# Kernel optimization log

Measured on AMD Instinct MI355X. Metric: run time of the kernel, lower is better.

## Reference

```python
import jax, jax.numpy as jnp
import numpy as np

N, D, H, DK, DEG = 8192, 512, 8, 64, 16
E = N * DEG
M = N


def setup_inputs() -> dict:
    key = jax.random.key(0)
    ks = jax.random.split(key, 12)
    x = jax.random.normal(ks[0], (N, D), dtype=jnp.float32)
    # every node has DEG neighbors -> sorted row index, random cols
    row_index = jnp.repeat(jnp.arange(N, dtype=jnp.int64), DEG)
    col_index = jax.random.randint(ks[1], (E,), 0, M, dtype=jnp.int64)
    to_col_index = jax.random.randint(ks[2], (M,), 0, N, dtype=jnp.int64)
    att_bias = 0.1 * jax.random.normal(ks[3], (H, E), dtype=jnp.float32)
    pos = 10.0 * jax.random.uniform(ks[4], (N, 3), dtype=jnp.float32)
    col_pos = 10.0 * jax.random.uniform(ks[5], (M, 3), dtype=jnp.float32)
    dist = jnp.linalg.norm(col_pos[col_index] - pos[row_index], axis=-1)
    s = 1.0 / np.sqrt(D)
    Wq = s * jax.random.normal(ks[6], (H, DK, D), dtype=jnp.float32)
    Wqv = s * jax.random.normal(ks[7], (H, 3, D), dtype=jnp.float32)
    Wk = s * jax.random.normal(ks[8], (H, DK, D), dtype=jnp.float32)
    Wv = s * jax.random.normal(ks[9], (H, DK, D), dtype=jnp.float32)
    Wout = s * jax.random.normal(ks[10], (D, D + 4 * H), dtype=jnp.float32)
    bout = jnp.zeros((D,), dtype=jnp.float32)
    return {"x": x, "row_index": row_index, "col_index": col_index,
            "to_col_index": to_col_index, "att_bias": att_bias, "dist": dist,
            "pos": pos, "col_pos": col_pos, "Wq": Wq, "Wqv": Wqv, "Wk": Wk,
            "Wv": Wv, "Wout": Wout, "bout": bout}


def reference(x, row_index, col_index, to_col_index, att_bias, dist, pos,
              col_pos, Wq, Wqv, Wk, Wv, Wout, bout):
    n = x.shape[0]
    dk = Wq.shape[1]
    scale = 1.0 / jnp.sqrt(jnp.asarray(dk, x.dtype))
    # per-head projections: [H, N, dk]
    q = jnp.einsum('nd,hkd->hnk', x, Wq) * scale
    qv = jnp.einsum('nd,hkd->hnk', x, Wqv)              # [H, N, 3]
    kx = jnp.einsum('nd,hkd->hnk', x, Wk)[:, to_col_index]  # [H, M, dk]
    vx = jnp.einsum('nd,hkd->hnk', x, Wv)[:, to_col_index]
    # gather per edge -> [E, H, *]
    qe = q[:, row_index].transpose(1, 0, 2)
    ke = kx[:, col_index].transpose(1, 0, 2)
    qve = qv[:, row_index].transpose(1, 0, 2)           # [E, H, 3]
    rel = col_pos[col_index] - pos[row_index]           # [E, 3]
    dist_e = jnp.where(dist == 0, jnp.inf, dist)        # masked_fill(dist==0, inf)
    # angular = qv_row . col_pos_col - qv_row . pos_row = qv_row . rel
    angular = jnp.einsum('ehc,ec->eh', qve, rel)
    logit = jnp.einsum('ehk,ehk->eh', qe, ke) + att_bias.T + angular / dist_e[:, None]
    # sparse (per-row segment) softmax
    m = jax.ops.segment_max(logit, row_index, num_segments=n)
    p = jnp.exp(logit - m[row_index])
    s = jax.ops.segment_sum(p, row_index, num_segments=n)
    att = p / s[row_index]                              # [E, H]
    natt = att / dist_e[:, None]
    dst_vec = jax.ops.segment_sum(natt[:, :, None] * col_pos[col_index][:, None, :],
                                  row_index, num_segments=n)   # [N, H, 3]
    avg_inv_dist = jax.ops.segment_sum(natt, row_index, num_segments=n)  # [N, H]
    src_vec = avg_inv_dist[:, :, None] * pos[:, None, :]
    diff = dst_vec - src_vec
    feat3 = diff / jnp.maximum(jnp.linalg.norm(diff, axis=-1, keepdims=True), 1e-12)
    ve = vx[:, col_index].transpose(1, 0, 2)            # [E, H, dk]
    y = jax.ops.segment_sum(att[:, :, None] * ve, row_index, num_segments=n)  # [N, H, dk]
    feat = jnp.concatenate([y, feat3, avg_inv_dist[:, :, None]], axis=-1)
    feat = feat.reshape(n, -1)                          # [N, H*(dk+4)]
    return feat @ Wout.T + bout
```

## Files before the change

### kernel.cpp

```cpp
#include <hip/hip_runtime.h>
#include <math.h>

#define N_NODES 8192
#define D_FEAT  512
#define DEG     16
#define E_EDGES (N_NODES * DEG)
#define FEAT_W  576
#define FEAT_USED 544
#define OUT_W   512
#define QKV_W   1664

typedef unsigned short u16;
typedef __attribute__((ext_vector_type(8))) short short8;
typedef __attribute__((ext_vector_type(8))) unsigned short us8;
typedef __attribute__((ext_vector_type(4))) float f32x4;

__device__ __forceinline__ u16 f2bf(float f) {
    union { float f; unsigned u; } c; c.f = f;
    unsigned u = c.u;
    unsigned r = u + 0x7FFFu + ((u >> 16) & 1u);
    return (u16)(r >> 16);
}
__device__ __forceinline__ float bf2f(u16 h) {
    union { unsigned u; float f; } c; c.u = ((unsigned)h) << 16;
    return c.f;
}

__device__ __forceinline__ void async16(const void* g, void* l) {
    __builtin_amdgcn_global_load_lds(
        (const __attribute__((address_space(1))) void*)g,
        (__attribute__((address_space(3))) void*)l, 16, 0, 0);
}

__device__ __forceinline__ us8 pack8(float4 a, float4 b, float s) {
    us8 w;
    w[0] = f2bf(a.x * s); w[1] = f2bf(a.y * s);
    w[2] = f2bf(a.z * s); w[3] = f2bf(a.w * s);
    w[4] = f2bf(b.x * s); w[5] = f2bf(b.y * s);
    w[6] = f2bf(b.z * s); w[7] = f2bf(b.w * s);
    return w;
}

__global__ __launch_bounds__(256) void gemm_qkv(
    const float* __restrict__ x,
    const float* __restrict__ Wq, const float* __restrict__ Wk,
    const float* __restrict__ Wv, const float* __restrict__ Wqv,
    u16* __restrict__ qkv)
{
    __shared__ u16 smem[128 * 64 * 2];
    u16* sA = smem;
    u16* sB = smem + 128 * 64;

    const int tid = threadIdx.x;
    const int flat = blockIdx.x;
    const int xcd = flat & 7;
    const int rr  = flat >> 3;
    const int bm  = (xcd + 8 * (rr / 13)) * 128;
    const int bn  = (rr % 13) * 128;

    const int wave = tid >> 6;
    const int lane = tid & 63;
    const int wr   = (wave >> 1) * 64;
    const int wc   = (wave & 1) * 64;
    const int lrow = lane & 15;
    const int quad = lane >> 4;

    f32x4 acc[4][4];
    #pragma unroll
    for (int i = 0; i < 4; ++i)
        #pragma unroll
        for (int j = 0; j < 4; ++j) {
            f32x4 z = {0.f, 0.f, 0.f, 0.f};
            acc[i][j] = z;
        }

    for (int k0 = 0; k0 < 512; k0 += 64) {
        #pragma unroll
        for (int i = 0; i < 4; ++i) {
            const int lin = i * 256 + tid;
            const int row = lin >> 3;
            const int seg = ((lin & 7) ^ (row & 7)) << 3;
            {
                const float* s = x + (size_t)(bm + row) * 512 + k0 + seg;
                const float4 a0 = *(const float4*)(s);
                const float4 a1 = *(const float4*)(s + 4);
                *(us8*)&sA[lin << 3] = pack8(a0, a1, 1.f);
            }
            {
                const int br = bn + row;
                const float* s = nullptr; float sc = 1.f;
                if (br < 512)       { s = Wq + (size_t)br * 512; sc = 0.125f; }
                else if (br < 1024) { s = Wk + (size_t)(br - 512) * 512; }
                else if (br < 1536) { s = Wv + (size_t)(br - 1024) * 512; }
                else if (br < 1560) { s = Wqv + (size_t)(br - 1536) * 512; }
                us8 w = {0, 0, 0, 0, 0, 0, 0, 0};
                if (s) {
                    const float4 b0 = *(const float4*)(s + k0 + seg);
                    const float4 b1 = *(const float4*)(s + k0 + seg + 4);
                    w = pack8(b0, b1, sc);
                }
                *(us8*)&sB[lin << 3] = w;
            }
        }
        __syncthreads();

        #pragma unroll
        for (int ko = 0; ko < 64; ko += 32) {
            const int cbase = ko >> 3;
            short8 a_h[4], b_h[4];
            #pragma unroll
            for (int t = 0; t < 4; ++t) {
                const int ra = wr + t * 16 + lrow;
                const int rb = wc + t * 16 + lrow;
                a_h[t] = *(const short8*)&sA[ra * 64 + (((cbase + quad) ^ (ra & 7)) << 3)];
                b_h[t] = *(const short8*)&sB[rb * 64 + (((cbase + quad) ^ (rb & 7)) << 3)];
            }
            #pragma unroll
            for (int mt = 0; mt < 4; ++mt)
                #pragma unroll
                for (int nt = 0; nt < 4; ++nt)
                    acc[mt][nt] = __builtin_amdgcn_mfma_f32_16x16x32_bf16(
                        a_h[mt], b_h[nt], acc[mt][nt], 0, 0, 0);
        }
        __syncthreads();
    }

    #pragma unroll
    for (int nt = 0; nt < 4; ++nt) {
        const int col = bn + wc + nt * 16 + lrow;
        #pragma unroll
        for (int mt = 0; mt < 4; ++mt)
            #pragma unroll
            for (int r = 0; r < 4; ++r) {
                const int row = bm + wr + mt * 16 + quad * 4 + r;
                qkv[(size_t)row * QKV_W + col] = f2bf(acc[mt][nt][r]);
            }
    }
}

__global__ __launch_bounds__(256) void gemm_out(
    const u16* __restrict__ feat, const float* __restrict__ Wout,
    const float* __restrict__ bout, float* __restrict__ out)
{
    __shared__ u16 smem[128 * 64 * 2];
    u16* sA = smem;
    u16* sB = smem + 128 * 64;

    const int tid = threadIdx.x;
    const int flat = blockIdx.x;
    const int xcd = flat & 7;
    const int rr  = flat >> 3;
    const int bm  = (xcd + 8 * (rr / 4)) * 128;
    const int bn  = (rr % 4) * 128;

    const int wave = tid >> 6;
    const int lane = tid & 63;
    const int wr   = (wave >> 1) * 64;
    const int wc   = (wave & 1) * 64;
    const int lrow = lane & 15;
    const int quad = lane >> 4;

    f32x4 acc[4][4];
    #pragma unroll
    for (int i = 0; i < 4; ++i)
        #pragma unroll
        for (int j = 0; j < 4; ++j) {
            f32x4 z = {0.f, 0.f, 0.f, 0.f};
            acc[i][j] = z;
        }

    for (int k0 = 0; k0 < FEAT_W; k0 += 64) {
        #pragma unroll
        for (int i = 0; i < 4; ++i) {
            const int lin = i * 256 + tid;
            const int row = lin >> 3;
            const int seg = ((lin & 7) ^ (row & 7)) << 3;
            async16(feat + (size_t)(bm + row) * FEAT_W + k0 + seg, sA + (lin << 3));
            {
                const int col = k0 + seg;
                us8 w = {0, 0, 0, 0, 0, 0, 0, 0};
                if (col < FEAT_USED) {
                    const float* s = Wout + (size_t)(bn + row) * FEAT_USED + col;
                    const float4 b0 = *(const float4*)(s);
                    const float4 b1 = *(const float4*)(s + 4);
                    w = pack8(b0, b1, 1.f);
                }
                *(us8*)&sB[lin << 3] = w;
            }
        }
        __syncthreads();

        #pragma unroll
        for (int ko = 0; ko < 64; ko += 32) {
            const int cbase = ko >> 3;
            short8 a_h[4], b_h[4];
            #pragma unroll
            for (int t = 0; t < 4; ++t) {
                const int ra = wr + t * 16 + lrow;
                const int rb = wc + t * 16 + lrow;
                a_h[t] = *(const short8*)&sA[ra * 64 + (((cbase + quad) ^ (ra & 7)) << 3)];
                b_h[t] = *(const short8*)&sB[rb * 64 + (((cbase + quad) ^ (rb & 7)) << 3)];
            }
            #pragma unroll
            for (int mt = 0; mt < 4; ++mt)
                #pragma unroll
                for (int nt = 0; nt < 4; ++nt)
                    acc[mt][nt] = __builtin_amdgcn_mfma_f32_16x16x32_bf16(
                        a_h[mt], b_h[nt], acc[mt][nt], 0, 0, 0);
        }
        __syncthreads();
    }

    #pragma unroll
    for (int nt = 0; nt < 4; ++nt) {
        const int col = bn + wc + nt * 16 + lrow;
        const float bb = bout[col];
        #pragma unroll
        for (int mt = 0; mt < 4; ++mt)
            #pragma unroll
            for (int r = 0; r < 4; ++r) {
                const int row = bm + wr + mt * 16 + quad * 4 + r;
                out[(size_t)row * OUT_W + col] = acc[mt][nt][r] + bb;
            }
    }
}

#define EK_WAVES 2
__global__ __launch_bounds__(EK_WAVES * 64) void edge_kernel(
    const u16* __restrict__ qkv,
    const int* __restrict__ col_index, const int* __restrict__ to_col,
    const float* __restrict__ att_bias, const float* __restrict__ dist,
    const float* __restrict__ pos, const float* __restrict__ col_pos,
    u16* __restrict__ feat)
{
    __shared__ u16 vbuf[EK_WAVES * DEG * 512];

    const int wave = threadIdx.x >> 6;
    const int lane = threadIdx.x & 63;
    const int n = blockIdx.x * EK_WAVES + wave;
    const int h = lane >> 3;
    const int sub = lane & 7;

    const size_t qbase = (size_t)n * QKV_W;
    const int hoff = lane * 8;

    float qf[8];
    {
        const us8 qu = *(const us8*)(qkv + qbase + hoff);
        #pragma unroll
        for (int i = 0; i < 8; ++i) qf[i] = bf2f(qu[i]);
    }
    float qv0, qv1, qv2;
    {
        const float qvl = bf2f(qkv[qbase + 1536 + (lane < 24 ? lane : 0)]);
        qv0 = __shfl(qvl, h * 3 + 0);
        qv1 = __shfl(qvl, h * 3 + 1);
        qv2 = __shfl(qvl, h * 3 + 2);
    }
    const float px = pos[3 * n + 0], py = pos[3 * n + 1], pz = pos[3 * n + 2];

    const int j16 = lane & 15;
    const int e0  = n * DEG + j16;
    const int c_l  = col_index[e0];
    const int cc_l = to_col[c_l];
    const float d_l = dist[e0];
    const float invd_l = (d_l == 0.f) ? 0.f : (1.f / d_l);
    const float rx_l = col_pos[3 * c_l + 0] - px;
    const float ry_l = col_pos[3 * c_l + 1] - py;
    const float rz_l = col_pos[3 * c_l + 2] - pz;

    const float b0 = att_bias[(size_t)h * E_EDGES + n * DEG + sub * 2 + 0];
    const float b1 = att_bias[(size_t)h * E_EDGES + n * DEG + sub * 2 + 1];

    float logit[DEG];
    u16* vb = &vbuf[wave * DEG * 512];
    #pragma unroll
    for (int j = 0; j < DEG; ++j) {
        const int cc = __shfl(cc_l, j);
        const u16* rowp = qkv + (size_t)cc * QKV_W + hoff;
        async16(rowp + 1024, vb + j * 512);
        const us8 ku = *(const us8*)(rowp + 512);
        float dot = 0.f;
        #pragma unroll
        for (int i = 0; i < 8; ++i) dot += qf[i] * bf2f(ku[i]);
        dot += __shfl_xor(dot, 1, 8);
        dot += __shfl_xor(dot, 2, 8);
        dot += __shfl_xor(dot, 4, 8);
        const float invd = __shfl(invd_l, j);
        const float ang = qv0 * __shfl(rx_l, j) + qv1 * __shfl(ry_l, j)
                        + qv2 * __shfl(rz_l, j);
        const float bj = __shfl((j & 1) ? b1 : b0, j >> 1, 8);
        logit[j] = dot + bj + ang * invd;
    }

    float m = logit[0];
    #pragma unroll
    for (int j = 1; j < DEG; ++j) m = fmaxf(m, logit[j]);
    float s = 0.f;
    #pragma unroll
    for (int j = 0; j < DEG; ++j) { logit[j] = __expf(logit[j] - m); s += logit[j]; }
    const float inv_s = 1.f / s;

    __syncthreads();

    float y[8] = {0.f, 0.f, 0.f, 0.f, 0.f, 0.f, 0.f, 0.f};
    float dx = 0.f, dy = 0.f, dz = 0.f, aid = 0.f;
    #pragma unroll
    for (int j = 0; j < DEG; ++j) {
        const float a = logit[j] * inv_s;
        const us8 vu = *(const us8*)&vb[j * 512 + hoff];
        #pragma unroll
        for (int i = 0; i < 8; ++i) y[i] += a * bf2f(vu[i]);
        const float na = a * __shfl(invd_l, j);
        dx += na * __shfl(rx_l, j);
        dy += na * __shfl(ry_l, j);
        dz += na * __shfl(rz_l, j);
        aid += na;
    }

    u16* f = feat + (size_t)n * FEAT_W + h * 68;
    ushort4 o0, o1;
    o0.x = f2bf(y[0]); o0.y = f2bf(y[1]); o0.z = f2bf(y[2]); o0.w = f2bf(y[3]);
    o1.x = f2bf(y[4]); o1.y = f2bf(y[5]); o1.z = f2bf(y[6]); o1.w = f2bf(y[7]);
    *(ushort4*)(f + sub * 8 + 0) = o0;
    *(ushort4*)(f + sub * 8 + 4) = o1;
    if (sub == 0) {
        const float nrm = sqrtf(dx * dx + dy * dy + dz * dz);
        const float rn = 1.f / fmaxf(nrm, 1e-12f);
        ushort4 ex;
        ex.x = f2bf(dx * rn); ex.y = f2bf(dy * rn);
        ex.z = f2bf(dz * rn); ex.w = f2bf(aid);
        *(ushort4*)(f + 64) = ex;
    }
}

extern "C" void kernel_launch(void* const* d_in, const int* in_sizes, int n_in,
                              void* d_out, int out_size, void* d_ws, size_t ws_size,
                              hipStream_t stream)
{
    const float* x         = (const float*)d_in[0];
    const int*   col_index = (const int*)d_in[2];
    const int*   to_col    = (const int*)d_in[3];
    const float* att_bias  = (const float*)d_in[4];
    const float* dist      = (const float*)d_in[5];
    const float* pos       = (const float*)d_in[6];
    const float* col_pos   = (const float*)d_in[7];
    const float* Wq        = (const float*)d_in[8];
    const float* Wqv       = (const float*)d_in[9];
    const float* Wk        = (const float*)d_in[10];
    const float* Wv        = (const float*)d_in[11];
    const float* Wout      = (const float*)d_in[12];
    const float* bout      = (const float*)d_in[13];
    float* out = (float*)d_out;

    char* ws = (char*)d_ws;
    u16* qkv  = (u16*)(ws + 0);
    u16* feat = (u16*)(ws + 27262976);

    dim3 blk(256);

    hipLaunchKernelGGL(gemm_qkv, dim3(64 * 13), blk, 0, stream,
                       x, Wq, Wk, Wv, Wqv, qkv);

    hipLaunchKernelGGL(edge_kernel, dim3(N_NODES / EK_WAVES), dim3(EK_WAVES * 64),
                       0, stream,
                       qkv, col_index, to_col, att_bias, dist, pos, col_pos, feat);

    hipLaunchKernelGGL(gemm_out, dim3(64 * 4), blk, 0, stream,
                       feat, Wout, bout, out);
}
```

Measured before the change: 197.6 us.

## Pre-convert GEMM operands to bf16 in a prep kernel and use async LDS loads

Adds a prep kernel that converts x, the fused Wq/Wk/Wv matrix and a zero-padded Wout to bf16 once per call. It also computes the small qv projection in fp32 there, so the QKV GEMM drops from 13 to 12 column tiles. Both GEMMs now stream bf16 tiles straight into LDS with global_load_lds instead of loading fp32 and converting in registers, which cuts redundant per-tile conversion and halves operand bytes. gemm_out uses 64-row M tiles to double its block count from 256 to 512. The cost is an extra launch and an extra round trip of the bf16 copies through memory.

```diff
diff --git a/kernel.cpp b/kernel.cpp
--- a/kernel.cpp
+++ b/kernel.cpp
@@ -8,7 +8,7 @@
 #define FEAT_W  576
 #define FEAT_USED 544
 #define OUT_W   512
-#define QKV_W   1664
+#define QKV_W   1536
 
 typedef unsigned short u16;
 typedef __attribute__((ext_vector_type(8))) short short8;
@@ -32,19 +32,8 @@
         (__attribute__((address_space(3))) void*)l, 16, 0, 0);
 }
 
-__device__ __forceinline__ us8 pack8(float4 a, float4 b, float s) {
-    us8 w;
-    w[0] = f2bf(a.x * s); w[1] = f2bf(a.y * s);
-    w[2] = f2bf(a.z * s); w[3] = f2bf(a.w * s);
-    w[4] = f2bf(b.x * s); w[5] = f2bf(b.y * s);
-    w[6] = f2bf(b.z * s); w[7] = f2bf(b.w * s);
-    return w;
-}
-
 __global__ __launch_bounds__(256) void gemm_qkv(
-    const float* __restrict__ x,
-    const float* __restrict__ Wq, const float* __restrict__ Wk,
-    const float* __restrict__ Wv, const float* __restrict__ Wqv,
+    const u16* __restrict__ xh, const u16* __restrict__ Bfuse,
     u16* __restrict__ qkv)
 {
     __shared__ u16 smem[128 * 64 * 2];
@@ -55,8 +44,8 @@
     const int flat = blockIdx.x;
     const int xcd = flat & 7;
     const int rr  = flat >> 3;
-    const int bm  = (xcd + 8 * (rr / 13)) * 128;
-    const int bn  = (rr % 13) * 128;
+    const int bm  = (xcd + 8 * (rr / 12)) * 128;
+    const int bn  = (rr % 12) * 128;
 
     const int wave = tid >> 6;
     const int lane = tid & 63;
@@ -80,27 +69,8 @@
             const int lin = i * 256 + tid;
             const int row = lin >> 3;
             const int seg = ((lin & 7) ^ (row & 7)) << 3;
-            {
-                const float* s = x + (size_t)(bm + row) * 512 + k0 + seg;
-                const float4 a0 = *(const float4*)(s);
-                const float4 a1 = *(const float4*)(s + 4);
-                *(us8*)&sA[lin << 3] = pack8(a0, a1, 1.f);
-            }
-            {
-                const int br = bn + row;
-                const float* s = nullptr; float sc = 1.f;
-                if (br < 512)       { s = Wq + (size_t)br * 512; sc = 0.125f; }
-                else if (br < 1024) { s = Wk + (size_t)(br - 512) * 512; }
-                else if (br < 1536) { s = Wv + (size_t)(br - 1024) * 512; }
-                else if (br < 1560) { s = Wqv + (size_t)(br - 1536) * 512; }
-                us8 w = {0, 0, 0, 0, 0, 0, 0, 0};
-                if (s) {
-                    const float4 b0 = *(const float4*)(s + k0 + seg);
-                    const float4 b1 = *(const float4*)(s + k0 + seg + 4);
-                    w = pack8(b0, b1, sc);
-                }
-                *(us8*)&sB[lin << 3] = w;
-            }
+            async16(xh    + (size_t)(bm + row) * 512 + k0 + seg, sA + (lin << 3));
+            async16(Bfuse + (size_t)(bn + row) * 512 + k0 + seg, sB + (lin << 3));
         }
         __syncthreads();
 
@@ -139,30 +109,30 @@
 }
 
 __global__ __launch_bounds__(256) void gemm_out(
-    const u16* __restrict__ feat, const float* __restrict__ Wout,
+    const u16* __restrict__ feat, const u16* __restrict__ Woth,
     const float* __restrict__ bout, float* __restrict__ out)
 {
-    __shared__ u16 smem[128 * 64 * 2];
+    __shared__ u16 smem[64 * 64 + 128 * 64];
     u16* sA = smem;
-    u16* sB = smem + 128 * 64;
+    u16* sB = smem + 64 * 64;
 
     const int tid = threadIdx.x;
     const int flat = blockIdx.x;
     const int xcd = flat & 7;
     const int rr  = flat >> 3;
-    const int bm  = (xcd + 8 * (rr / 4)) * 128;
+    const int bm  = (xcd + 8 * (rr / 4)) * 64;
     const int bn  = (rr % 4) * 128;
 
     const int wave = tid >> 6;
     const int lane = tid & 63;
-    const int wr   = (wave >> 1) * 64;
+    const int wr   = (wave >> 1) * 32;
     const int wc   = (wave & 1) * 64;
     const int lrow = lane & 15;
     const int quad = lane >> 4;
 
-    f32x4 acc[4][4];
-    #pragma unroll
-    for (int i = 0; i < 4; ++i)
+    f32x4 acc[2][4];
+    #pragma unroll
+    for (int i = 0; i < 2; ++i)
         #pragma unroll
         for (int j = 0; j < 4; ++j) {
             f32x4 z = {0.f, 0.f, 0.f, 0.f};
@@ -170,39 +140,38 @@
         }
 
     for (int k0 = 0; k0 < FEAT_W; k0 += 64) {
+        #pragma unroll
+        for (int i = 0; i < 2; ++i) {
+            const int lin = i * 256 + tid;
+            const int row = lin >> 3;
+            const int seg = ((lin & 7) ^ (row & 7)) << 3;
+            async16(feat + (size_t)(bm + row) * FEAT_W + k0 + seg, sA + (lin << 3));
+        }
         #pragma unroll
         for (int i = 0; i < 4; ++i) {
             const int lin = i * 256 + tid;
             const int row = lin >> 3;
             const int seg = ((lin & 7) ^ (row & 7)) << 3;
-            async16(feat + (size_t)(bm + row) * FEAT_W + k0 + seg, sA + (lin << 3));
-            {
-                const int col = k0 + seg;
-                us8 w = {0, 0, 0, 0, 0, 0, 0, 0};
-                if (col < FEAT_USED) {
-                    const float* s = Wout + (size_t)(bn + row) * FEAT_USED + col;
-                    const float4 b0 = *(const float4*)(s);
-                    const float4 b1 = *(const float4*)(s + 4);
-                    w = pack8(b0, b1, 1.f);
-                }
-                *(us8*)&sB[lin << 3] = w;
-            }
+            async16(Woth + (size_t)(bn + row) * FEAT_W + k0 + seg, sB + (lin << 3));
         }
         __syncthreads();
 
         #pragma unroll
         for (int ko = 0; ko < 64; ko += 32) {
             const int cbase = ko >> 3;
-            short8 a_h[4], b_h[4];
+            short8 a_h[2], b_h[4];
+            #pragma unroll
+            for (int t = 0; t < 2; ++t) {
+                const int ra = wr + t * 16 + lrow;
+                a_h[t] = *(const short8*)&sA[ra * 64 + (((cbase + quad) ^ (ra & 7)) << 3)];
+            }
             #pragma unroll
             for (int t = 0; t < 4; ++t) {
-                const int ra = wr + t * 16 + lrow;
                 const int rb = wc + t * 16 + lrow;
-                a_h[t] = *(const short8*)&sA[ra * 64 + (((cbase + quad) ^ (ra & 7)) << 3)];
                 b_h[t] = *(const short8*)&sB[rb * 64 + (((cbase + quad) ^ (rb & 7)) << 3)];
             }
             #pragma unroll
-            for (int mt = 0; mt < 4; ++mt)
+            for (int mt = 0; mt < 2; ++mt)
                 #pragma unroll
                 for (int nt = 0; nt < 4; ++nt)
                     acc[mt][nt] = __builtin_amdgcn_mfma_f32_16x16x32_bf16(
@@ -216,7 +185,7 @@
         const int col = bn + wc + nt * 16 + lrow;
         const float bb = bout[col];
         #pragma unroll
-        for (int mt = 0; mt < 4; ++mt)
+        for (int mt = 0; mt < 2; ++mt)
             #pragma unroll
             for (int r = 0; r < 4; ++r) {
                 const int row = bm + wr + mt * 16 + quad * 4 + r;
@@ -225,9 +194,65 @@
     }
 }
 
+__global__ __launch_bounds__(256) void prep_kernel(
+    const float* __restrict__ x,
+    const float* __restrict__ Wq, const float* __restrict__ Wk,
+    const float* __restrict__ Wv, const float* __restrict__ Wqv,
+    const float* __restrict__ Wout,
+    u16* __restrict__ xh, u16* __restrict__ B, u16* __restrict__ Woth,
+    float* __restrict__ qv_all)
+{
+    const int b = blockIdx.x;
+    const int tid = threadIdx.x;
+    if (b < 4096) {
+        const int i = b * 256 + tid;
+        const float4 v = ((const float4*)x)[i];
+        ushort4 h;
+        h.x = f2bf(v.x); h.y = f2bf(v.y); h.z = f2bf(v.z); h.w = f2bf(v.w);
+        ((ushort4*)xh)[i] = h;
+    } else if (b < 4864) {
+        const int idx = (b - 4096) * 256 + tid;
+        const int row = idx >> 7;
+        const int c4  = idx & 127;
+        const float* src; float scale = 1.f;
+        if (row < 512)       { src = Wq + (size_t)row * 512; scale = 0.125f; }
+        else if (row < 1024) { src = Wk + (size_t)(row - 512) * 512; }
+        else                 { src = Wv + (size_t)(row - 1024) * 512; }
+        const float4 v = *(const float4*)(src + c4 * 4);
+        ushort4 h;
+        h.x = f2bf(v.x * scale); h.y = f2bf(v.y * scale);
+        h.z = f2bf(v.z * scale); h.w = f2bf(v.w * scale);
+        ((ushort4*)B)[idx] = h;
+    } else if (b < 5152) {
+        const int i = (b - 4864) * 256 + tid;
+        const int row = i / (FEAT_W / 4);
+        const int c4  = i % (FEAT_W / 4);
+        float4 v = make_float4(0.f, 0.f, 0.f, 0.f);
+        if (c4 < FEAT_USED / 4)
+            v = *(const float4*)(Wout + (size_t)row * FEAT_USED + c4 * 4);
+        ushort4 h;
+        h.x = f2bf(v.x); h.y = f2bf(v.y); h.z = f2bf(v.z); h.w = f2bf(v.w);
+        ((ushort4*)Woth)[i] = h;
+    } else {
+        const int t = (b - 5152) * 256 + tid;
+        const int n = t / 24;
+        const int c = t % 24;
+        const float4* xr = (const float4*)(x + (size_t)n * 512);
+        const float4* wr = (const float4*)(Wqv + (size_t)c * 512);
+        float acc = 0.f;
+        #pragma unroll 4
+        for (int k = 0; k < 128; ++k) {
+            const float4 a = xr[k], w = wr[k];
+            acc += a.x * w.x + a.y * w.y + a.z * w.z + a.w * w.w;
+        }
+        qv_all[t] = acc;
+    }
+}
+
 #define EK_WAVES 2
 __global__ __launch_bounds__(EK_WAVES * 64) void edge_kernel(
     const u16* __restrict__ qkv,
+    const float* __restrict__ qv_all,
     const int* __restrict__ col_index, const int* __restrict__ to_col,
     const float* __restrict__ att_bias, const float* __restrict__ dist,
     const float* __restrict__ pos, const float* __restrict__ col_pos,
@@ -252,7 +277,7 @@
     }
     float qv0, qv1, qv2;
     {
-        const float qvl = bf2f(qkv[qbase + 1536 + (lane < 24 ? lane : 0)]);
+        const float qvl = qv_all[n * 24 + (lane < 24 ? lane : 0)];
         qv0 = __shfl(qvl, h * 3 + 0);
         qv1 = __shfl(qvl, h * 3 + 1);
         qv2 = __shfl(qvl, h * 3 + 2);
@@ -354,18 +379,25 @@
     float* out = (float*)d_out;
 
     char* ws = (char*)d_ws;
-    u16* qkv  = (u16*)(ws + 0);
-    u16* feat = (u16*)(ws + 27262976);
+    u16*   qkv    = (u16*)(ws + 0);
+    u16*   xh     = (u16*)(ws + 25165824);
+    u16*   Bfuse  = (u16*)(ws + 33554432);
+    u16*   Woth   = (u16*)(ws + 35127296);
+    float* qv_all = (float*)(ws + 35717120);
+    u16*   feat   = (u16*)(ws + 36503552);
 
     dim3 blk(256);
 
-    hipLaunchKernelGGL(gemm_qkv, dim3(64 * 13), blk, 0, stream,
-                       x, Wq, Wk, Wv, Wqv, qkv);
+    hipLaunchKernelGGL(prep_kernel, dim3(5920), blk, 0, stream,
+                       x, Wq, Wk, Wv, Wqv, Wout, xh, Bfuse, Woth, qv_all);
+
+    hipLaunchKernelGGL(gemm_qkv, dim3(768), blk, 0, stream, xh, Bfuse, qkv);
 
     hipLaunchKernelGGL(edge_kernel, dim3(N_NODES / EK_WAVES), dim3(EK_WAVES * 64),
                        0, stream,
-                       qkv, col_index, to_col, att_bias, dist, pos, col_pos, feat);
-
-    hipLaunchKernelGGL(gemm_out, dim3(64 * 4), blk, 0, stream,
-                       feat, Wout, bout, out);
-}
+                       qkv, qv_all, col_index, to_col, att_bias, dist, pos,
+                       col_pos, feat);
+
+    hipLaunchKernelGGL(gemm_out, dim3(512), blk, 0, stream,
+                       feat, Woth, bout, out);
+}
```

Measured after the change: 291.5 us. +47.5%, slower.
